# Kernel optimization log

Hardware: AMD Instinct MI355X
Metric: run time of the kernel (lower is better)

Reference implementation:

```python
import jax, jax.numpy as jnp
import numpy as np

S, B = 64, 256
CH_IN, CH_OUT, AUX, HID = 128, 128, 3, 32
EPS = 1e-5


def _ln(h, g, b):
    mu = jnp.mean(h, axis=-1, keepdims=True)
    var = jnp.mean(jnp.square(h - mu), axis=-1, keepdims=True)
    return (h - mu) * jax.lax.rsqrt(var + EPS) * g + b


def _hyper_mlp(z, W1, b1, g1, be1, W2, b2, g2, be2, W3, b3):
    # Linear -> LN -> ReLU -> Linear -> LN -> ReLU -> Linear (droprate=0)
    h = jax.nn.relu(_ln(jnp.einsum('sba,ha->sbh', z, W1) + b1, g1, be1))
    h = jax.nn.relu(_ln(jnp.einsum('sbh,kh->sbk', h, W2) + b2, g2, be2))
    return jnp.einsum('sbh,oh->sbo', h, W3) + b3


def setup_inputs() -> dict:
    key = jax.random.key(0)
    ks = jax.random.split(key, 24)
    f = lambda k, shp: (jax.random.normal(k, shp, dtype=jnp.float32) * 0.05)
    inp = {
        'x': jax.random.normal(ks[0], (S, B, CH_IN), dtype=jnp.float32),
        'z': jax.random.normal(ks[1], (S, B, AUX), dtype=jnp.float32),
        # weight-branch hypernet params
        'wW1': f(ks[2], (HID, AUX)), 'wb1': jnp.zeros((HID,), jnp.float32),
        'wg1': jnp.ones((HID,), jnp.float32), 'wbe1': jnp.zeros((HID,), jnp.float32),
        'wW2': f(ks[3], (HID, HID)), 'wb2': jnp.zeros((HID,), jnp.float32),
        'wg2': jnp.ones((HID,), jnp.float32), 'wbe2': jnp.zeros((HID,), jnp.float32),
        'wW3': f(ks[4], (CH_OUT * CH_IN, HID)), 'wb3': jnp.zeros((CH_OUT * CH_IN,), jnp.float32),
        # bias-branch hypernet params
        'bW1': f(ks[5], (HID, AUX)), 'bb1': jnp.zeros((HID,), jnp.float32),
        'bg1': jnp.ones((HID,), jnp.float32), 'bbe1': jnp.zeros((HID,), jnp.float32),
        'bW2': f(ks[6], (HID, HID)), 'bb2': jnp.zeros((HID,), jnp.float32),
        'bg2': jnp.ones((HID,), jnp.float32), 'bbe2': jnp.zeros((HID,), jnp.float32),
        'bW3': f(ks[7], (CH_OUT, HID)), 'bb3': jnp.zeros((CH_OUT,), jnp.float32),
    }
    return inp


def reference(x, z,
              wW1, wb1, wg1, wbe1, wW2, wb2, wg2, wbe2, wW3, wb3,
              bW1, bb1, bg1, bbe1, bW2, bb2, bg2, bbe2, bW3, bb3):
    # per-token weight: [S,B,ch_out*ch_in] -> [S,B,ch_out,ch_in]
    weight = _hyper_mlp(z, wW1, wb1, wg1, wbe1, wW2, wb2, wg2, wbe2, wW3, wb3)
    weight = weight.reshape(S, B, CH_OUT, CH_IN)
    bias = _hyper_mlp(z, bW1, bb1, bg1, bbe1, bW2, bb2, bg2, bbe2, bW3, bb3)
    # batched mat-vec: out[s,b,o] = sum_i weight[s,b,o,i] * x[s,b,i] + bias
    out = jnp.einsum('sboi,sbi->sbo', weight, x) + bias
    return out
```

## Files before the change

kernel.cpp:

```cpp
#include <hip/hip_runtime.h>
#include <hip/hip_fp16.h>
#include <stdint.h>

#define T_DIM   16384
#define NKS     67
#define LN_EPS  1e-5f

typedef _Float16 f16;
typedef __attribute__((ext_vector_type(2))) _Float16 h2v;
typedef __attribute__((ext_vector_type(4))) _Float16 h4v;
typedef __attribute__((ext_vector_type(8))) _Float16 h8v;
typedef __attribute__((ext_vector_type(4))) float    f32x4;

union H2U { uint32_t u; h2v h; };
union H8U { uint32_t u[4]; h8v v; };

__global__ __launch_bounds__(256) void prep_hyper(
    const float* __restrict__ x, const float* __restrict__ z,
    const float* __restrict__ wW1, const float* __restrict__ wb1,
    const float* __restrict__ wg1, const float* __restrict__ wbe1,
    const float* __restrict__ wW2, const float* __restrict__ wb2,
    const float* __restrict__ wg2, const float* __restrict__ wbe2,
    const float* __restrict__ bW1, const float* __restrict__ bb1,
    const float* __restrict__ bg1, const float* __restrict__ bbe1,
    const float* __restrict__ bW2, const float* __restrict__ bb2,
    const float* __restrict__ bg2, const float* __restrict__ bbe2,
    const float* __restrict__ wW3, const float* __restrict__ wb3,
    const float* __restrict__ bW3,
    f16* __restrict__ w3p, f16* __restrict__ xf,
    f16* __restrict__ h2w, f16* __restrict__ h2b)
{
  const int tid = threadIdx.x;
  const int bid = blockIdx.x;

  if (bid < 268) {
    const int idx  = bid * 256 + tid;
    const int lane = idx & 63;
    int rest = idx >> 6;
    const int n  = rest & 1;  rest >>= 1;
    const int i2 = rest & 1;  rest >>= 1;
    const int ks = rest % 67;
    const int os = rest / 67;

    const int o     = os * 32 + n * 16 + (lane & 15);
    const int slice = ks * 2 + i2;
    const int h0    = (lane >> 4) * 8;

    float v[8];
    if (slice < 133) {
      const float* src;
      if      (slice < 128) src = wW3 + ((size_t)o * 128 + slice) * 32 + h0;
      else if (slice < 132) src = wb3 + (size_t)o * 128 + (slice - 128) * 32 + h0;
      else                  src = bW3 + (size_t)o * 32 + h0;
      float4 a = *(const float4*)src;
      float4 b = *(const float4*)(src + 4);
      v[0]=a.x; v[1]=a.y; v[2]=a.z; v[3]=a.w; v[4]=b.x; v[5]=b.y; v[6]=b.z; v[7]=b.w;
    } else {
#pragma unroll
      for (int j = 0; j < 8; ++j) v[j] = 0.f;
    }
    h8v pk;
#pragma unroll
    for (int j = 0; j < 8; ++j) pk[j] = (f16)v[j];
    *(h8v*)(w3p + ((size_t)rest * 2048 + i2 * 1024 + n * 512 + lane * 8)) = pk;
    return;
  }

  const int hb = bid - 268;

  {
    const size_t base = (size_t)hb * 16384;
#pragma unroll
    for (int u = 0; u < 16; ++u) {
      const size_t off = base + u * 1024 + tid * 4;
      float4 a = *(const float4*)(x + off);
      h4v p; p[0] = (f16)a.x; p[1] = (f16)a.y; p[2] = (f16)a.z; p[3] = (f16)a.w;
      *(h4v*)(xf + off) = p;
    }
  }

  const int br  = hb >> 6;
  const int tok = (hb & 63) * 256 + tid;
  const float* W1  = br ? bW1  : wW1;  const float* b1  = br ? bb1  : wb1;
  const float* g1  = br ? bg1  : wg1;  const float* be1 = br ? bbe1 : wbe1;
  const float* W2  = br ? bW2  : wW2;  const float* b2  = br ? bb2  : wb2;
  const float* g2  = br ? bg2  : wg2;  const float* be2 = br ? bbe2 : wbe2;
  f16* dst = (br ? h2b : h2w) + (size_t)tok * 32;

  const float z0 = z[tok * 3 + 0], z1 = z[tok * 3 + 1], z2 = z[tok * 3 + 2];

  float h1[32];
  float s = 0.f, s2 = 0.f;
#pragma unroll
  for (int j = 0; j < 32; ++j) {
    float v = W1[j * 3] * z0 + W1[j * 3 + 1] * z1 + W1[j * 3 + 2] * z2 + b1[j];
    h1[j] = v; s += v; s2 += v * v;
  }
  float mu  = s * (1.f / 32.f);
  float var = fmaxf(s2 * (1.f / 32.f) - mu * mu, 0.f);
  float rr  = rsqrtf(var + LN_EPS);
#pragma unroll
  for (int j = 0; j < 32; ++j)
    h1[j] = fmaxf((h1[j] - mu) * rr * g1[j] + be1[j], 0.f);

  float h2a[32];
  s = 0.f; s2 = 0.f;
#pragma unroll
  for (int j = 0; j < 32; ++j) {
    float acc = b2[j];
#pragma unroll
    for (int kk = 0; kk < 8; ++kk) {
      float4 w = *(const float4*)&W2[j * 32 + kk * 4];
      acc += w.x * h1[kk * 4] + w.y * h1[kk * 4 + 1]
           + w.z * h1[kk * 4 + 2] + w.w * h1[kk * 4 + 3];
    }
    h2a[j] = acc; s += acc; s2 += acc * acc;
  }
  mu  = s * (1.f / 32.f);
  var = fmaxf(s2 * (1.f / 32.f) - mu * mu, 0.f);
  rr  = rsqrtf(var + LN_EPS);
#pragma unroll
  for (int j8 = 0; j8 < 4; ++j8) {
    h8v pk;
#pragma unroll
    for (int j = 0; j < 8; ++j)
      pk[j] = (f16)fmaxf((h2a[j8*8+j] - mu) * rr * g2[j8*8+j] + be2[j8*8+j], 0.f);
    *(h8v*)(dst + j8 * 8) = pk;
  }
}

__global__ __launch_bounds__(1024, 4) void gemm_kernel(
    const f16* __restrict__ xf, const f16* __restrict__ w3p,
    const f16* __restrict__ h2w, const f16* __restrict__ h2b,
    const float* __restrict__ bb3, float* __restrict__ out)
{
  __shared__ __align__(16) f16 xs[64][136];
  __shared__ __align__(16) f32x4 red[3][4][8][64];

  const int tid   = threadIdx.x;
  const int lane  = tid & 63;
  const int wid   = tid >> 6;
  const int strip = wid & 3;
  const int q     = wid >> 2;
  const int lm    = lane & 15, hc = lane >> 4, hbase = hc * 8;
  const int t0    = blockIdx.x * 64;
  const int o0    = strip * 32;
  const int ks0   = q * 17;
  const int n_it  = (q == 3) ? 16 : 17;

  {
    const int r = tid >> 4, c = (tid & 15) * 8;
    *(h8v*)&xs[r][c] = *(const h8v*)(xf + (size_t)(t0 + r) * 128 + c);
  }

  uint32_t h2p[4][4];
#pragma unroll
  for (int m = 0; m < 4; ++m) {
    H8U c; c.v = *(const h8v*)(h2w + (size_t)(t0 + m * 16 + lm) * 32 + hbase);
#pragma unroll
    for (int qq = 0; qq < 4; ++qq) h2p[m][qq] = c.u[qq];
  }

  float bbv[2];
#pragma unroll
  for (int n = 0; n < 2; ++n)
    bbv[n] = (q == 0) ? bb3[o0 + n * 16 + lm] : 0.f;

  __syncthreads();

  const f16* bp = w3p + (size_t)(strip * 67 + ks0) * 2048 + lane * 8;

#define LOADSET(S) do { \
    S[0][0] = *(const h8v*)(bp); \
    S[0][1] = *(const h8v*)(bp + 512); \
    S[1][0] = *(const h8v*)(bp + 1024); \
    S[1][1] = *(const h8v*)(bp + 1536); \
    bp += 2048; } while (0)

  f32x4 acc[4][2];
#pragma unroll
  for (int m = 0; m < 4; ++m)
#pragma unroll
    for (int n = 0; n < 2; ++n) acc[m][n] = (f32x4){0.f, 0.f, 0.f, 0.f};

  auto STEP = [&](h8v (&bs)[2][2], int ks) {
    const int ksg = ks0 + ks;
    h8v af0[4], af1[4];
    if (__builtin_expect(ksg < 64, 1)) {
#pragma unroll
      for (int m = 0; m < 4; ++m) {
        const uint32_t xp = *(const uint32_t*)&xs[m * 16 + lm][2 * ksg];
        H2U x0, x1;
        x0.u = (xp & 0xffffu) | (xp << 16);
        x1.u = (xp >> 16) | (xp & 0xffff0000u);
        H8U r0, r1;
#pragma unroll
        for (int qq = 0; qq < 4; ++qq) {
          H2U hq; hq.u = h2p[m][qq];
          H2U p0; p0.h = x0.h * hq.h; r0.u[qq] = p0.u;
          H2U p1; p1.h = x1.h * hq.h; r1.u[qq] = p1.u;
        }
        af0[m] = r0.v; af1[m] = r1.v;
      }
    } else if (ksg < 66) {
      const int s = (ksg - 64) * 2;
#pragma unroll
      for (int m = 0; m < 4; ++m) {
        af0[m] = *(const h8v*)&xs[m * 16 + lm][s * 32 + hbase];
        af1[m] = *(const h8v*)&xs[m * 16 + lm][(s + 1) * 32 + hbase];
      }
    } else {
#pragma unroll
      for (int m = 0; m < 4; ++m) {
        af0[m] = *(const h8v*)(h2b + (size_t)(t0 + m * 16 + lm) * 32 + hbase);
        af1[m] = af0[m];
      }
    }
#pragma unroll
    for (int n = 0; n < 2; ++n)
#pragma unroll
      for (int m = 0; m < 4; ++m)
        acc[m][n] = __builtin_amdgcn_mfma_f32_16x16x32_f16(af0[m], bs[0][n], acc[m][n], 0, 0, 0);
#pragma unroll
    for (int n = 0; n < 2; ++n)
#pragma unroll
      for (int m = 0; m < 4; ++m)
        acc[m][n] = __builtin_amdgcn_mfma_f32_16x16x32_f16(af1[m], bs[1][n], acc[m][n], 0, 0, 0);
  };

  h8v bA[2][2], bB[2][2];
  LOADSET(bA);
  LOADSET(bB);

  int ks = 0;
#pragma unroll 1
  while (ks + 2 <= n_it) {
    STEP(bA, ks);
    if (ks + 2 < n_it) LOADSET(bA);
    STEP(bB, ks + 1);
    if (ks + 3 < n_it) LOADSET(bB);
    ks += 2;
  }
  if (ks < n_it) STEP(bA, ks);
#undef LOADSET

  if (q > 0) {
#pragma unroll
    for (int m = 0; m < 4; ++m)
#pragma unroll
      for (int n = 0; n < 2; ++n)
        red[q - 1][strip][m * 2 + n][lane] = acc[m][n];
  }
  __syncthreads();

  if (q == 0) {
#pragma unroll
    for (int m = 0; m < 4; ++m) {
#pragma unroll
      for (int n = 0; n < 2; ++n) {
        f32x4 r0 = red[0][strip][m * 2 + n][lane];
        f32x4 r1 = red[1][strip][m * 2 + n][lane];
        f32x4 r2 = red[2][strip][m * 2 + n][lane];
        f32x4 t  = acc[m][n] + r0 + r1 + r2;
        const int gc = o0 + n * 16 + lm;
#pragma unroll
        for (int r_ = 0; r_ < 4; ++r_) {
          const int row = t0 + m * 16 + hc * 4 + r_;
          out[(size_t)row * 128 + gc] = t[r_] + bbv[n];
        }
      }
    }
  }
}

extern "C" void kernel_launch(void* const* d_in, const int* in_sizes, int n_in,
                              void* d_out, int out_size, void* d_ws, size_t ws_size,
                              hipStream_t stream)
{
  const float* x    = (const float*)d_in[0];
  const float* z    = (const float*)d_in[1];
  const float* wW1  = (const float*)d_in[2];
  const float* wb1  = (const float*)d_in[3];
  const float* wg1  = (const float*)d_in[4];
  const float* wbe1 = (const float*)d_in[5];
  const float* wW2  = (const float*)d_in[6];
  const float* wb2  = (const float*)d_in[7];
  const float* wg2  = (const float*)d_in[8];
  const float* wbe2 = (const float*)d_in[9];
  const float* wW3  = (const float*)d_in[10];
  const float* wb3  = (const float*)d_in[11];
  const float* bW1  = (const float*)d_in[12];
  const float* bb1  = (const float*)d_in[13];
  const float* bg1  = (const float*)d_in[14];
  const float* bbe1 = (const float*)d_in[15];
  const float* bW2  = (const float*)d_in[16];
  const float* bb2  = (const float*)d_in[17];
  const float* bg2  = (const float*)d_in[18];
  const float* bbe2 = (const float*)d_in[19];
  const float* bW3  = (const float*)d_in[20];
  const float* bb3  = (const float*)d_in[21];

  uint8_t* ws = (uint8_t*)d_ws;
  f16* w3p = (f16*)ws;
  f16* xf  = (f16*)(ws + 1097728);
  f16* h2w = (f16*)(ws + 1097728 + 4194304);
  f16* h2b = (f16*)(ws + 1097728 + 4194304 + 1048576);
  float* outf = (float*)d_out;

  hipLaunchKernelGGL(prep_hyper, dim3(396), dim3(256), 0, stream,
                     x, z,
                     wW1, wb1, wg1, wbe1, wW2, wb2, wg2, wbe2,
                     bW1, bb1, bg1, bbe1, bW2, bb2, bg2, bbe2,
                     wW3, wb3, bW3,
                     w3p, xf, h2w, h2b);
  hipLaunchKernelGGL(gemm_kernel, dim3(256), dim3(1024), 0, stream,
                     xf, w3p, h2w, h2b, bb3, outf);
}
```

Baseline: 54.43 us.

## Split K across blocks with atomic output accumulation and pre-duplicated x in LDS

The GEMM kernel moves the K-split from warps inside a block to separate blocks: 512 blocks of 512 threads, each handling 128 tokens and a quarter of K. Partial results go straight to the output with atomicAdd instead of an LDS reduction plus syncthreads. The prep kernel gains extra blocks that zero the output first. x is stored in LDS already duplicated into half2 pairs so the inner loop skips the shuffle ops. The cost is four times the global atomic traffic on the output and an extra zeroing pass, traded for lower register and LDS pressure per block and no intra-block reduction.

```diff
diff --git a/kernel.cpp b/kernel.cpp
--- a/kernel.cpp
+++ b/kernel.cpp
@@ -3,7 +3,6 @@
 #include <stdint.h>
 
 #define T_DIM   16384
-#define NKS     67
 #define LN_EPS  1e-5f
 
 typedef _Float16 f16;
@@ -14,6 +13,7 @@
 
 union H2U { uint32_t u; h2v h; };
 union H8U { uint32_t u[4]; h8v v; };
+union H8S { h8v v; uint16_t s[8]; };
 
 __global__ __launch_bounds__(256) void prep_hyper(
     const float* __restrict__ x, const float* __restrict__ z,
@@ -28,10 +28,20 @@
     const float* __restrict__ wW3, const float* __restrict__ wb3,
     const float* __restrict__ bW3,
     f16* __restrict__ w3p, f16* __restrict__ xf,
-    f16* __restrict__ h2w, f16* __restrict__ h2b)
+    f16* __restrict__ h2w, f16* __restrict__ h2b,
+    float* __restrict__ outz)
 {
   const int tid = threadIdx.x;
   const int bid = blockIdx.x;
+
+  if (bid >= 396) {
+    float* dst = outz + (size_t)(bid - 396) * 16384 + tid * 4;
+    const float4 z4 = {0.f, 0.f, 0.f, 0.f};
+#pragma unroll
+    for (int u = 0; u < 16; ++u)
+      *(float4*)(dst + u * 1024) = z4;
+    return;
+  }
 
   if (bid < 268) {
     const int idx  = bid * 256 + tid;
@@ -129,44 +139,25 @@
   }
 }
 
-__global__ __launch_bounds__(1024, 4) void gemm_kernel(
+__global__ __launch_bounds__(512, 4) void gemm_kernel(
     const f16* __restrict__ xf, const f16* __restrict__ w3p,
     const f16* __restrict__ h2w, const f16* __restrict__ h2b,
     const float* __restrict__ bb3, float* __restrict__ out)
 {
-  __shared__ __align__(16) f16 xs[64][136];
-  __shared__ __align__(16) f32x4 red[3][4][8][64];
+  __shared__ uint32_t xd[128][130];
 
   const int tid   = threadIdx.x;
   const int lane  = tid & 63;
   const int wid   = tid >> 6;
+  const int wm    = wid >> 2;
   const int strip = wid & 3;
-  const int q     = wid >> 2;
   const int lm    = lane & 15, hc = lane >> 4, hbase = hc * 8;
-  const int t0    = blockIdx.x * 64;
+  const int tile  = blockIdx.x >> 2;
+  const int kh    = blockIdx.x & 3;
+  const int t0    = tile * 128;
   const int o0    = strip * 32;
-  const int ks0   = q * 17;
-  const int n_it  = (q == 3) ? 16 : 17;
-
-  {
-    const int r = tid >> 4, c = (tid & 15) * 8;
-    *(h8v*)&xs[r][c] = *(const h8v*)(xf + (size_t)(t0 + r) * 128 + c);
-  }
-
-  uint32_t h2p[4][4];
-#pragma unroll
-  for (int m = 0; m < 4; ++m) {
-    H8U c; c.v = *(const h8v*)(h2w + (size_t)(t0 + m * 16 + lm) * 32 + hbase);
-#pragma unroll
-    for (int qq = 0; qq < 4; ++qq) h2p[m][qq] = c.u[qq];
-  }
-
-  float bbv[2];
-#pragma unroll
-  for (int n = 0; n < 2; ++n)
-    bbv[n] = (q == 0) ? bb3[o0 + n * 16 + lm] : 0.f;
-
-  __syncthreads();
+  const int ks0   = kh * 17;
+  const int n_it  = (kh == 3) ? 16 : 17;
 
   const f16* bp = w3p + (size_t)(strip * 67 + ks0) * 2048 + lane * 8;
 
@@ -177,6 +168,41 @@
     S[1][1] = *(const h8v*)(bp + 1536); \
     bp += 2048; } while (0)
 
+  h8v bA[2][2], bB[2][2];
+  LOADSET(bA);
+  LOADSET(bB);
+
+  uint32_t h2p[4][4];
+#pragma unroll
+  for (int m = 0; m < 4; ++m) {
+    H8U c; c.v = *(const h8v*)(h2w + (size_t)(t0 + wm * 64 + m * 16 + lm) * 32 + hbase);
+#pragma unroll
+    for (int q = 0; q < 4; ++q) h2p[m][q] = c.u[q];
+  }
+
+  float bbv[2];
+#pragma unroll
+  for (int n = 0; n < 2; ++n)
+    bbv[n] = (kh == 0) ? bb3[o0 + n * 16 + lm] : 0.f;
+
+  {
+    const int r = tid >> 2, c0 = (tid & 3) * 32;
+    const f16* src = xf + (size_t)(t0 + r) * 128 + c0;
+#pragma unroll
+    for (int u = 0; u < 4; ++u) {
+      H8S hh; hh.v = *(const h8v*)(src + u * 8);
+#pragma unroll
+      for (int p = 0; p < 4; ++p) {
+        uint2 d;
+        d.x = (uint32_t)hh.s[p * 2]     * 0x10001u;
+        d.y = (uint32_t)hh.s[p * 2 + 1] * 0x10001u;
+        *(uint2*)&xd[r][c0 + u * 8 + p * 2] = d;
+      }
+    }
+  }
+
+  __syncthreads();
+
   f32x4 acc[4][2];
 #pragma unroll
   for (int m = 0; m < 4; ++m)
@@ -189,16 +215,14 @@
     if (__builtin_expect(ksg < 64, 1)) {
 #pragma unroll
       for (int m = 0; m < 4; ++m) {
-        const uint32_t xp = *(const uint32_t*)&xs[m * 16 + lm][2 * ksg];
-        H2U x0, x1;
-        x0.u = (xp & 0xffffu) | (xp << 16);
-        x1.u = (xp >> 16) | (xp & 0xffff0000u);
+        const uint2 xx = *(const uint2*)&xd[wm * 64 + m * 16 + lm][2 * ksg];
+        H2U x0, x1; x0.u = xx.x; x1.u = xx.y;
         H8U r0, r1;
 #pragma unroll
-        for (int qq = 0; qq < 4; ++qq) {
-          H2U hq; hq.u = h2p[m][qq];
-          H2U p0; p0.h = x0.h * hq.h; r0.u[qq] = p0.u;
-          H2U p1; p1.h = x1.h * hq.h; r1.u[qq] = p1.u;
+        for (int q = 0; q < 4; ++q) {
+          H2U hq; hq.u = h2p[m][q];
+          H2U p0; p0.h = x0.h * hq.h; r0.u[q] = p0.u;
+          H2U p1; p1.h = x1.h * hq.h; r1.u[q] = p1.u;
         }
         af0[m] = r0.v; af1[m] = r1.v;
       }
@@ -206,13 +230,14 @@
       const int s = (ksg - 64) * 2;
 #pragma unroll
       for (int m = 0; m < 4; ++m) {
-        af0[m] = *(const h8v*)&xs[m * 16 + lm][s * 32 + hbase];
-        af1[m] = *(const h8v*)&xs[m * 16 + lm][(s + 1) * 32 + hbase];
+        const f16* xr = xf + (size_t)(t0 + wm * 64 + m * 16 + lm) * 128;
+        af0[m] = *(const h8v*)(xr + s * 32 + hbase);
+        af1[m] = *(const h8v*)(xr + (s + 1) * 32 + hbase);
       }
     } else {
 #pragma unroll
       for (int m = 0; m < 4; ++m) {
-        af0[m] = *(const h8v*)(h2b + (size_t)(t0 + m * 16 + lm) * 32 + hbase);
+        af0[m] = *(const h8v*)(h2b + (size_t)(t0 + wm * 64 + m * 16 + lm) * 32 + hbase);
         af1[m] = af0[m];
       }
     }
@@ -227,10 +252,6 @@
       for (int m = 0; m < 4; ++m)
         acc[m][n] = __builtin_amdgcn_mfma_f32_16x16x32_f16(af1[m], bs[1][n], acc[m][n], 0, 0, 0);
   };
-
-  h8v bA[2][2], bB[2][2];
-  LOADSET(bA);
-  LOADSET(bB);
 
   int ks = 0;
 #pragma unroll 1
@@ -244,30 +265,15 @@
   if (ks < n_it) STEP(bA, ks);
 #undef LOADSET
 
-  if (q > 0) {
-#pragma unroll
-    for (int m = 0; m < 4; ++m)
-#pragma unroll
-      for (int n = 0; n < 2; ++n)
-        red[q - 1][strip][m * 2 + n][lane] = acc[m][n];
-  }
-  __syncthreads();
-
-  if (q == 0) {
-#pragma unroll
-    for (int m = 0; m < 4; ++m) {
-#pragma unroll
-      for (int n = 0; n < 2; ++n) {
-        f32x4 r0 = red[0][strip][m * 2 + n][lane];
-        f32x4 r1 = red[1][strip][m * 2 + n][lane];
-        f32x4 r2 = red[2][strip][m * 2 + n][lane];
-        f32x4 t  = acc[m][n] + r0 + r1 + r2;
-        const int gc = o0 + n * 16 + lm;
-#pragma unroll
-        for (int r_ = 0; r_ < 4; ++r_) {
-          const int row = t0 + m * 16 + hc * 4 + r_;
-          out[(size_t)row * 128 + gc] = t[r_] + bbv[n];
-        }
+#pragma unroll
+  for (int m = 0; m < 4; ++m) {
+#pragma unroll
+    for (int n = 0; n < 2; ++n) {
+      const int gc = o0 + n * 16 + lm;
+#pragma unroll
+      for (int r_ = 0; r_ < 4; ++r_) {
+        const int row = t0 + wm * 64 + m * 16 + hc * 4 + r_;
+        atomicAdd(&out[(size_t)row * 128 + gc], acc[m][n][r_] + bbv[n]);
       }
     }
   }
@@ -307,12 +313,12 @@
   f16* h2b = (f16*)(ws + 1097728 + 4194304 + 1048576);
   float* outf = (float*)d_out;
 
-  hipLaunchKernelGGL(prep_hyper, dim3(396), dim3(256), 0, stream,
+  hipLaunchKernelGGL(prep_hyper, dim3(524), dim3(256), 0, stream,
                      x, z,
                      wW1, wb1, wg1, wbe1, wW2, wb2, wg2, wbe2,
                      bW1, bb1, bg1, bbe1, bW2, bb2, bg2, bbe2,
                      wW3, wb3, bW3,
-                     w3p, xf, h2w, h2b);
-  hipLaunchKernelGGL(gemm_kernel, dim3(256), dim3(1024), 0, stream,
+                     w3p, xf, h2w, h2b, outf);
+  hipLaunchKernelGGL(gemm_kernel, dim3(512), dim3(512), 0, stream,
                      xf, w3p, h2w, h2b, bb3, outf);
 }
```

After: 79.29 us. +45.7%, slower.
